# Kernel tuning notes

Hardware: AMD Instinct MI355X
Metric: run time of the kernel (lower is better)

Reference implementation:

```python
import jax, jax.numpy as jnp
import numpy as np

N = 100000      # nodes
E = 1600000     # edges
DIN, DH, DOUT = 128, 256, 40


def setup_inputs() -> dict:
    key = jax.random.key(0)
    ks = jax.random.split(key, 24)

    def w(i, fan_in, fan_out):
        s = 1.0 / np.sqrt(fan_in)
        return jax.random.uniform(ks[i], (fan_in, fan_out), jnp.float32, -s, s)

    def b(i, fan_in, fan_out):
        s = 1.0 / np.sqrt(fan_in)
        return jax.random.uniform(ks[i], (fan_out,), jnp.float32, -s, s)

    return {
        "x": jax.random.normal(ks[0], (N, DIN), jnp.float32),
        "edge_index": jax.random.randint(ks[1], (2, E), 0, N, dtype=jnp.int64),
        # updates_continues: Linear(DIN,DH), Linear(DH,DH), Linear(DH,DOUT)
        "Wc0": w(2, DIN, DH),  "bc0": b(3, DIN, DH),
        "Wc1": w(4, DH, DH),   "bc1": b(5, DH, DH),
        "Wc2": w(6, DH, DOUT), "bc2": b(7, DH, DOUT),
        # updates_exit: Linear(DIN,DOUT) x2, Linear(DH,DOUT) x2
        "We0": w(8, DIN, DOUT),  "be0": b(9, DIN, DOUT),
        "We1": w(10, DIN, DOUT), "be1": b(11, DIN, DOUT),
        "We2": w(12, DH, DOUT),  "be2": b(13, DH, DOUT),
        "We3": w(14, DH, DOUT),  "be3": b(15, DH, DOUT),
    }


def _gcn_agg(h, src, dst):
    """Symmetric-normalized GCN aggregation with self-loops: D^-1/2 (A+I) D^-1/2 h."""
    ones = jnp.ones(src.shape[0], h.dtype)
    deg = jax.ops.segment_sum(ones, dst, num_segments=N) + 1.0  # self-loop
    dinv = jax.lax.rsqrt(deg)
    coef = dinv[src] * dinv[dst]                    # [E]
    msgs = h[src] * coef[:, None]                   # [E, d] gather
    out = jax.ops.segment_sum(msgs, dst, num_segments=N)  # scatter-add
    return out + h * (dinv * dinv)[:, None]         # self-loop term


def reference(x, edge_index, Wc0, bc0, Wc1, bc1, Wc2, bc2,
              We0, be0, We1, be1, We2, be2, We3, be3):
    src, dst = edge_index[0], edge_index[1]
    Wc = [(Wc0, bc0), (Wc1, bc1), (Wc2, bc2)]
    We = [(We0, be0), (We1, be1), (We2, be2), (We3, be3)]

    h = x
    outs = [jax.nn.log_softmax(h @ We[0][0] + We[0][1], axis=1)]
    for i in range(3):
        h = _gcn_agg(h, src, dst)
        outs.append(jax.nn.log_softmax(h @ We[i + 1][0] + We[i + 1][1], axis=1))
        h = h @ Wc[i][0] + Wc[i][1]
        if i < 2:
            h = jax.nn.relu(h)  # dropout is identity in eval mode
    return jnp.stack(outs, axis=1)  # [N, num_layers+1, DOUT]
```

## Files before the change

### kernel.cpp

```cpp
#include <hip/hip_runtime.h>

#define NNODES 100000
#define NEDGES 1600000
#define NBKT 782

typedef __attribute__((ext_vector_type(8))) short bf16x8;
typedef __attribute__((ext_vector_type(4))) float f32x4;
typedef __attribute__((ext_vector_type(2))) float f32x2;

__device__ __forceinline__ float bf2f(unsigned v) {
  union { unsigned u; float f; } x; x.u = v << 16; return x.f;
}
__device__ __forceinline__ unsigned short f2bf(float f) {
  union { float f; unsigned u; } x; x.f = f;
  unsigned r = x.u + 0x7fffu + ((x.u >> 16) & 1u);
  return (unsigned short)(r >> 16);
}
__device__ __forceinline__ f32x2 unpk(unsigned u) {
  union { unsigned q; float f; } lo, hi;
  lo.q = u << 16; hi.q = u & 0xffff0000u;
  f32x2 r; r.x = lo.f; r.y = hi.f; return r;
}
__device__ __forceinline__ unsigned short ldcv(const void* p, int i, int f32) {
  return f32 ? f2bf(((const float*)p)[i]) : ((const unsigned short*)p)[i];
}
__device__ __forceinline__ int detect_i64(const int* __restrict__ ei) {
  int lane = threadIdx.x & 63;
  int hv = ei[2 * lane + 1];
  unsigned long long nz = __ballot(hv != 0);
  return (__popcll(nz) < 4) ? 1 : 0;
}
__device__ __forceinline__ int edge_at(const int* __restrict__ ei, int j, int i64) {
  return i64 ? ei[2 * j] : ei[j];
}

__global__ void k_zero(int* __restrict__ p, int n) {
  int v = blockIdx.x * blockDim.x + threadIdx.x;
  if (v < n) p[v] = 0;
}


__global__ __launch_bounds__(256) void k_bcnt(const int* __restrict__ ei,
                                              int* __restrict__ bcnt,
                                              const unsigned* __restrict__ xw,
                                              int* __restrict__ flags) {
  __shared__ int h[NBKT];
  __shared__ int cF;
  int t = threadIdx.x;
  for (int i = t; i < NBKT; i += 256) h[i] = 0;
  if (blockIdx.x == 0 && t == 0) cF = 0;
  __syncthreads();
  if (blockIdx.x == 0) {
    int hf = 0;
    for (int i = t; i < 2048; i += 256) {
      unsigned lo = xw[i] & 0xffffu;
      unsigned e = (lo >> 7) & 0xffu;
      if (e >= 0xC0u) hf++;
    }
    atomicAdd(&cF, hf);
  }
  int i64 = detect_i64(ei);
  int e0 = blockIdx.x * 4096;
#pragma unroll
  for (int k = 0; k < 16; ++k) {
    int e = e0 + t + k * 256;
    if (e < NEDGES) {
      int d = edge_at(ei, NEDGES + e, i64);
      if ((unsigned)d < NNODES) atomicAdd(&h[d >> 7], 1);
    }
  }
  __syncthreads();
  for (int i = t; i < NBKT; i += 256)
    if (h[i]) atomicAdd(&bcnt[i], h[i]);
  if (blockIdx.x == 0 && t == 0) flags[0] = (cF > 32) ? 1 : 0;
}

__global__ void k_bscan2(const int* __restrict__ bcnt, int* __restrict__ bbase,
                         int* __restrict__ gcur) {
  int l = threadIdx.x;
  int v[13];
  int s = 0;
#pragma unroll
  for (int k = 0; k < 13; ++k) {
    int j = l * 13 + k;
    v[k] = (j < NBKT) ? bcnt[j] : 0;
    s += v[k];
  }
  int x = s;
#pragma unroll
  for (int o = 1; o < 64; o <<= 1) {
    int y = __shfl_up(x, o, 64);
    if (l >= o) x += y;
  }
  int excl = x - s;
#pragma unroll
  for (int k = 0; k < 13; ++k) {
    int j = l * 13 + k;
    if (j < NBKT) { bbase[j] = excl; gcur[j] = excl; }
    excl += v[k];
  }
  if (l == 63) bbase[NBKT] = x;
}

__global__ __launch_bounds__(256) void k_bstage(const int* __restrict__ ei,
                                                int* __restrict__ gcur,
                                                int* __restrict__ stage) {
  __shared__ int h[NBKT];
  __shared__ int base[NBKT];
  int t = threadIdx.x;
  for (int i = t; i < NBKT; i += 256) h[i] = 0;
  __syncthreads();
  int i64 = detect_i64(ei);
  int e0 = blockIdx.x * 4096;
  int bkt[16], lp[16], rec[16];
#pragma unroll
  for (int k = 0; k < 16; ++k) {
    bkt[k] = -1;
    int e = e0 + t + k * 256;
    if (e < NEDGES) {
      int d = edge_at(ei, NEDGES + e, i64);
      if ((unsigned)d < NNODES) {
        int s = edge_at(ei, e, i64);
        if ((unsigned)s >= NNODES) s = NNODES - 1;
        bkt[k] = d >> 7;
        rec[k] = ((d & 127) << 17) | s;
        lp[k] = atomicAdd(&h[bkt[k]], 1);
      }
    }
  }
  __syncthreads();
  for (int i = t; i < NBKT; i += 256)
    base[i] = h[i] ? atomicAdd(&gcur[i], h[i]) : 0;
  __syncthreads();
#pragma unroll
  for (int k = 0; k < 16; ++k)
    if (bkt[k] >= 0) stage[base[bkt[k]] + lp[k]] = rec[k];
}

__global__ __launch_bounds__(256) void k_bplace(const int* __restrict__ stage,
                                                const int* __restrict__ bbase,
                                                int* __restrict__ offs,
                                                float* __restrict__ dinv,
                                                int* __restrict__ csr_src) {
  __shared__ int h[128];
  __shared__ int cur[128];
  int b = blockIdx.x;
  int t = threadIdx.x;
  int n0 = b * 128;
  int NN = NNODES - n0; if (NN > 128) NN = 128;
  int s0 = bbase[b], s1 = bbase[b + 1];
  int cnt = s1 - s0;
  if (t < 128) h[t] = 0;
  __syncthreads();
  for (int i = t; i < cnt; i += 256) {
    int rec = stage[s0 + i];
    atomicAdd(&h[rec >> 17], 1);
  }
  __syncthreads();
  if (t < 64) {
    int a = h[2 * t], c = h[2 * t + 1];
    int s = a + c;
    int x = s;
#pragma unroll
    for (int o = 1; o < 64; o <<= 1) {
      int y = __shfl_up(x, o, 64);
      if (t >= o) x += y;
    }
    int excl = s0 + x - s;
    cur[2 * t] = excl;
    cur[2 * t + 1] = excl + a;
    if (2 * t < NN) {
      offs[n0 + 2 * t] = excl;
      dinv[n0 + 2 * t] = rsqrtf((float)a + 1.0f);
    }
    if (2 * t + 1 < NN) {
      offs[n0 + 2 * t + 1] = excl + a;
      dinv[n0 + 2 * t + 1] = rsqrtf((float)c + 1.0f);
    }
  }
  if (b == NBKT - 1 && t == 0) offs[NNODES] = s1;
  __syncthreads();
  for (int i = t; i < cnt; i += 256) {
    int rec = stage[s0 + i];
    int pos = atomicAdd(&cur[rec >> 17], 1);
    csr_src[pos] = rec & 0x1FFFF;
  }
}

struct CvtP {
  const void* src[7];
  unsigned short* dst[7];
  int n[7];
  const void* W[6];
  unsigned short* WT[6];
};

__global__ void k_cvt(CvtP p, const int* __restrict__ flags,
                      const float* __restrict__ dinv, unsigned short* __restrict__ xs) {
  int a = blockIdx.y;
  int f32 = flags[0];
  if (a < 7) {
    int n = p.n[a];
    const float* sf = (const float*)p.src[a];
    const unsigned short* sb = (const unsigned short*)p.src[a];
    unsigned short* d = p.dst[a];
    for (int i = blockIdx.x * blockDim.x + threadIdx.x; i < n; i += gridDim.x * blockDim.x) {
      if (a == 0) {
        float v = f32 ? sf[i] : bf2f((unsigned)sb[i]);
        d[i] = f32 ? f2bf(v) : sb[i];
        xs[i] = f2bf(v * dinv[i >> 7]);
      } else {
        d[i] = f32 ? f2bf(sf[i]) : sb[i];
      }
    }
  } else {
    int g = blockIdx.x * 256 + threadIdx.x;
    if (g < 32768) {
      int k = g >> 8, c = g & 255;
      p.WT[0][c * 128 + k] = ldcv(p.W[0], g, f32);
    } else if (g < 98304) {
      int l = g - 32768; int k = l >> 8, c = l & 255;
      p.WT[1][c * 256 + k] = ldcv(p.W[1], l, f32);
    } else if (g < 104448) {
      int l = g - 98304; int c = l >> 7, k = l & 127;
      p.WT[2][l] = (c < 40) ? ldcv(p.W[2], k * 40 + c, f32) : (unsigned short)0;
    } else if (g < 110592) {
      int l = g - 104448; int c = l >> 7, k = l & 127;
      p.WT[3][l] = (c < 40) ? ldcv(p.W[3], k * 40 + c, f32) : (unsigned short)0;
    } else if (g < 122880) {
      int l = g - 110592; int c = l >> 8, k = l & 255;
      p.WT[4][l] = (c < 40) ? ldcv(p.W[4], k * 40 + c, f32) : (unsigned short)0;
    } else if (g < 135168) {
      int l = g - 122880; int c = l >> 8, k = l & 255;
      p.WT[5][l] = (c < 40) ? ldcv(p.W[5], k * 40 + c, f32) : (unsigned short)0;
    }
  }
}

__device__ __forceinline__ void accp(f32x2 (&acc)[4], uint4 u, float w) {
  acc[0] += unpk(u.x) * w;
  acc[1] += unpk(u.y) * w;
  acc[2] += unpk(u.z) * w;
  acc[3] += unpk(u.w) * w;
}

template <int D, int EPB>
__global__ __launch_bounds__(256) void k_agg(
    const unsigned short* __restrict__ hin, unsigned short* __restrict__ hout,
    const int* __restrict__ offs, const int* __restrict__ csr_src,
    const float* __restrict__ dinv) {
  constexpr int LPR = D / 8;
  constexpr int R = 64 / LPR;
  constexpr int NB = EPB / R;
  const int lane = threadIdx.x & 63;
  const int g = lane / LPR;
  const int l = lane % LPR;
  const int v = (blockIdx.x * 256 + threadIdx.x) >> 6;
  if (v >= NNODES) return;

  float dv = dinv[v];
  const size_t vbase = (size_t)v * D + l * 8;
  uint4 su = *(const uint4*)(hin + vbase);
  f32x2 acc[4];
#pragma unroll
  for (int k = 0; k < 4; ++k) acc[k] = (f32x2)0.f;
  accp(acc, su, (g == 0) ? 1.f : 0.f);

  int b0 = offs[v];
  int n = offs[v + 1] - b0;
  if (n > 0) {
    int s[NB];
    float wg[NB];
#pragma unroll
    for (int j = 0; j < NB; ++j) {
      int e = j * R + g;
      int ec = (e < n) ? e : (n - 1);
      s[j] = csr_src[b0 + ec];
      wg[j] = (e < n) ? 1.f : 0.f;
    }
    for (int i = 0; i < n; i += EPB) {
      uint4 gu[NB];
#pragma unroll
      for (int j = 0; j < NB; ++j)
        gu[j] = *(const uint4*)(hin + (size_t)s[j] * D + l * 8);
      float wc[NB];
#pragma unroll
      for (int j = 0; j < NB; ++j) wc[j] = wg[j];
      int i2 = i + EPB;
#pragma unroll
      for (int j = 0; j < NB; ++j) {
        int e = i2 + j * R + g;
        int ec = (e < n) ? e : (n - 1);
        s[j] = csr_src[b0 + ec];
        wg[j] = (e < n) ? 1.f : 0.f;
      }
#pragma unroll
      for (int j = 0; j < NB; ++j) accp(acc, gu[j], wc[j]);
    }
  }
  float a8[8];
#pragma unroll
  for (int k = 0; k < 4; ++k) { a8[2 * k] = acc[k].x; a8[2 * k + 1] = acc[k].y; }
#pragma unroll
  for (int k = 0; k < 8; ++k) {
#pragma unroll
    for (int o = LPR; o < 64; o <<= 1) a8[k] += __shfl_xor(a8[k], o, 64);
  }
  if (g == 0) {
    uint4 ov;
    ov.x = (unsigned)f2bf(dv * a8[0]) | ((unsigned)f2bf(dv * a8[1]) << 16);
    ov.y = (unsigned)f2bf(dv * a8[2]) | ((unsigned)f2bf(dv * a8[3]) << 16);
    ov.z = (unsigned)f2bf(dv * a8[4]) | ((unsigned)f2bf(dv * a8[5]) << 16);
    ov.w = (unsigned)f2bf(dv * a8[6]) | ((unsigned)f2bf(dv * a8[7]) << 16);
    *(uint4*)(hout + vbase) = ov;
  }
}

__global__ __launch_bounds__(256) void k_agg40(
    const unsigned short* __restrict__ P, const int* __restrict__ offs,
    const int* __restrict__ csr_src, const float* __restrict__ dinv,
    const unsigned short* __restrict__ bias, float* __restrict__ outp) {
  const int lane = threadIdx.x & 63;
  const int g = lane >> 5, l = lane & 31;
  const bool act = l < 20;
  const int v = (blockIdx.x * 256 + threadIdx.x) >> 6;
  if (v >= NNODES) return;

  float dv = dinv[v];
  f32x2 a = (f32x2)0.f;
  if (act && g == 0) a = unpk(*(const unsigned*)(P + (size_t)v * 40 + l * 2));
  int b0 = offs[v];
  int n = offs[v + 1] - b0;
  if (n > 0) {
    int s[4];
    float wg[4];
#pragma unroll
    for (int j = 0; j < 4; ++j) {
      int e = j * 2 + g;
      int ec = (e < n) ? e : (n - 1);
      s[j] = csr_src[b0 + ec];
      wg[j] = (e < n) ? 1.f : 0.f;
    }
    for (int i = 0; i < n; i += 8) {
      unsigned gu[4];
#pragma unroll
      for (int j = 0; j < 4; ++j)
        gu[j] = act ? *(const unsigned*)(P + (size_t)s[j] * 40 + l * 2) : 0u;
      float wc[4];
#pragma unroll
      for (int j = 0; j < 4; ++j) wc[j] = wg[j];
      int i2 = i + 8;
#pragma unroll
      for (int j = 0; j < 4; ++j) {
        int e = i2 + j * 2 + g;
        int ec = (e < n) ? e : (n - 1);
        s[j] = csr_src[b0 + ec];
        wg[j] = (e < n) ? 1.f : 0.f;
      }
#pragma unroll
      for (int j = 0; j < 4; ++j) a += unpk(gu[j]) * wc[j];
    }
  }
  a.x += __shfl_xor(a.x, 32, 64);
  a.y += __shfl_xor(a.y, 32, 64);
  float a0 = 0.f, a1 = 0.f;
  if (act) {
    a0 = dv * a.x + bf2f((unsigned)bias[l * 2]);
    a1 = dv * a.y + bf2f((unsigned)bias[l * 2 + 1]);
  }
  float m = act ? fmaxf(a0, a1) : -1e30f;
#pragma unroll
  for (int o = 16; o > 0; o >>= 1) m = fmaxf(m, __shfl_xor(m, o, 32));
  float ss = act ? (expf(a0 - m) + expf(a1 - m)) : 0.f;
#pragma unroll
  for (int o = 16; o > 0; o >>= 1) ss += __shfl_xor(ss, o, 32);
  float ls = logf(ss) + m;
  if (act && g == 0) {
    float2 o2;
    o2.x = a0 - ls;
    o2.y = a1 - ls;
    *(float2*)(outp + (size_t)v * 160 + l * 2) = o2;
  }
}

template <int K, bool SCALE>
__device__ __forceinline__ void mlp_body(
    char* smem, int m0, int c0,
    const unsigned short* __restrict__ A, const unsigned short* __restrict__ WT,
    const unsigned short* __restrict__ bias, unsigned short* __restrict__ out,
    const float* __restrict__ dinv) {
  short* As = (short*)smem;
  short* Bs = (short*)(smem + 10240);
  const int t = threadIdx.x;
  const int lane = t & 63, wv = t >> 6;
  const int mw = (wv >> 1) * 64, nw = (wv & 1) * 64;
  const int lr = lane & 15, lq = lane >> 4;

  f32x4 acc[4][4];
#pragma unroll
  for (int i = 0; i < 4; ++i)
#pragma unroll
    for (int j = 0; j < 4; ++j) acc[i][j] = (f32x4)0.f;

  for (int kc = 0; kc < K; kc += 32) {
    __syncthreads();
#pragma unroll
    for (int it = 0; it < 2; ++it) {
      int idx = t + it * 256;
      int row = idx >> 2, seg = idx & 3;
      uint4 u = make_uint4(0, 0, 0, 0);
      int gr = m0 + row;
      if (gr < NNODES) u = *(const uint4*)(A + (size_t)gr * K + kc + seg * 8);
      *(uint4*)&As[row * 40 + seg * 8] = u;
      uint4 v = *(const uint4*)(WT + (size_t)(c0 + row) * K + kc + seg * 8);
      *(uint4*)&Bs[row * 40 + seg * 8] = v;
    }
    __syncthreads();
    bf16x8 af[4], bfr[4];
#pragma unroll
    for (int i = 0; i < 4; ++i)
      af[i] = *(const bf16x8*)&As[(mw + 16 * i + lr) * 40 + lq * 8];
#pragma unroll
    for (int j = 0; j < 4; ++j)
      bfr[j] = *(const bf16x8*)&Bs[(nw + 16 * j + lr) * 40 + lq * 8];
#pragma unroll
    for (int i = 0; i < 4; ++i)
#pragma unroll
      for (int j = 0; j < 4; ++j)
        acc[i][j] = __builtin_amdgcn_mfma_f32_16x16x32_bf16(af[i], bfr[j], acc[i][j], 0, 0, 0);
  }

  float bv[4];
#pragma unroll
  for (int j = 0; j < 4; ++j) bv[j] = bf2f((unsigned)bias[c0 + nw + 16 * j + lr]);
#pragma unroll
  for (int i = 0; i < 4; ++i) {
    int rbase = m0 + mw + 16 * i + lq * 4;
#pragma unroll
    for (int r = 0; r < 4; ++r) {
      int row = rbase + r;
      if (row < NNODES) {
        float s = SCALE ? dinv[row] : 1.f;
#pragma unroll
        for (int j = 0; j < 4; ++j) {
          int col = c0 + nw + 16 * j + lr;
          float v = fmaxf(acc[i][j][r] + bv[j], 0.f) * s;
          out[(size_t)row * 256 + col] = f2bf(v);
        }
      }
    }
  }
}

template <int K, bool SOFTMAX>
__device__ __forceinline__ void exit_body(
    char* smem, int m0,
    const unsigned short* __restrict__ A, const unsigned short* __restrict__ WT,
    const unsigned short* __restrict__ bias, float* __restrict__ outp,
    unsigned short* __restrict__ Pout, const float* __restrict__ dinv) {
  constexpr int KP = K + 8;
  short* As = (short*)smem;
  short* Bs = (short*)(smem + 10240);
  const int t = threadIdx.x;
  const int lane = t & 63, wv = t >> 6;
  const int mw = wv * 32;
  const int lr = lane & 15, lq = lane >> 4;

  for (int idx = t; idx < 48 * (K / 8); idx += 256) {
    int row = idx / (K / 8), seg = idx % (K / 8);
    uint4 w = *(const uint4*)(WT + (size_t)row * K + seg * 8);
    *(uint4*)&Bs[row * KP + seg * 8] = w;
  }

  f32x4 acc[2][3];
#pragma unroll
  for (int i = 0; i < 2; ++i)
#pragma unroll
    for (int j = 0; j < 3; ++j) acc[i][j] = (f32x4)0.f;

  for (int kc = 0; kc < K; kc += 32) {
    __syncthreads();
#pragma unroll
    for (int it = 0; it < 2; ++it) {
      int idx = t + it * 256;
      int row = idx >> 2, seg = idx & 3;
      uint4 u = make_uint4(0, 0, 0, 0);
      int gr = m0 + row;
      if (gr < NNODES) u = *(const uint4*)(A + (size_t)gr * K + kc + seg * 8);
      *(uint4*)&As[row * 40 + seg * 8] = u;
    }
    __syncthreads();
    bf16x8 af[2], bfr[3];
#pragma unroll
    for (int i = 0; i < 2; ++i)
      af[i] = *(const bf16x8*)&As[(mw + 16 * i + lr) * 40 + lq * 8];
#pragma unroll
    for (int j = 0; j < 3; ++j)
      bfr[j] = *(const bf16x8*)&Bs[(16 * j + lr) * KP + kc + lq * 8];
#pragma unroll
    for (int i = 0; i < 2; ++i)
#pragma unroll
      for (int j = 0; j < 3; ++j)
        acc[i][j] = __builtin_amdgcn_mfma_f32_16x16x32_bf16(af[i], bfr[j], acc[i][j], 0, 0, 0);
  }

  if (SOFTMAX) {
    float bv0 = bf2f((unsigned)bias[lr]);
    float bv1 = bf2f((unsigned)bias[16 + lr]);
    float bv2 = (lr < 8) ? bf2f((unsigned)bias[32 + lr]) : 0.f;
#pragma unroll
    for (int i = 0; i < 2; ++i) {
#pragma unroll
      for (int r = 0; r < 4; ++r) {
        int row = m0 + mw + 16 * i + lq * 4 + r;
        float v0 = acc[i][0][r] + bv0;
        float v1 = acc[i][1][r] + bv1;
        float v2 = (lr < 8) ? (acc[i][2][r] + bv2) : -1e30f;
        float m = fmaxf(fmaxf(v0, v1), v2);
#pragma unroll
        for (int o = 8; o > 0; o >>= 1) m = fmaxf(m, __shfl_xor(m, o, 16));
        float ss = expf(v0 - m) + expf(v1 - m) + ((lr < 8) ? expf(v2 - m) : 0.f);
#pragma unroll
        for (int o = 8; o > 0; o >>= 1) ss += __shfl_xor(ss, o, 16);
        float ls = logf(ss) + m;
        if (row < NNODES) {
          outp[(size_t)row * 160 + lr] = v0 - ls;
          outp[(size_t)row * 160 + 16 + lr] = v1 - ls;
          if (lr < 8) outp[(size_t)row * 160 + 32 + lr] = v2 - ls;
        }
      }
    }
  } else {
#pragma unroll
    for (int i = 0; i < 2; ++i) {
#pragma unroll
      for (int r = 0; r < 4; ++r) {
        int row = m0 + mw + 16 * i + lq * 4 + r;
        if (row < NNODES) {
          float s = dinv[row];
          Pout[(size_t)row * 40 + lr] = f2bf(acc[i][0][r] * s);
          Pout[(size_t)row * 40 + 16 + lr] = f2bf(acc[i][1][r] * s);
          if (lr < 8) Pout[(size_t)row * 40 + 32 + lr] = f2bf(acc[i][2][r] * s);
        }
      }
    }
  }
}

template <int K> struct ExitSM { static constexpr int B = 10240 + 48 * (K + 8) * 2; };

__global__ __launch_bounds__(256) void k_exit0(
    const unsigned short* __restrict__ A, const unsigned short* __restrict__ WT,
    const unsigned short* __restrict__ bias, float* __restrict__ outp,
    const float* __restrict__ dinv) {
  __shared__ __align__(16) char smem[ExitSM<128>::B];
  exit_body<128, true>(smem, blockIdx.x * 128, A, WT, bias, outp, nullptr, dinv);
}

__global__ __launch_bounds__(256) void k_exit3(
    const unsigned short* __restrict__ A, const unsigned short* __restrict__ WT,
    unsigned short* __restrict__ Pout, const float* __restrict__ dinv) {
  __shared__ __align__(16) char smem[ExitSM<256>::B];
  exit_body<256, false>(smem, blockIdx.x * 128, A, WT, nullptr, nullptr, Pout, dinv);
}

template <int K, bool MLPSCALE>
__global__ __launch_bounds__(256) void k_exit_mlp(
    const unsigned short* __restrict__ A,
    const unsigned short* __restrict__ WTmlp, const unsigned short* __restrict__ bmlp,
    unsigned short* __restrict__ outmlp,
    const unsigned short* __restrict__ WTex, const unsigned short* __restrict__ bex,
    float* __restrict__ outp, const float* __restrict__ dinv) {
  constexpr int SM = (ExitSM<K>::B > 20480) ? ExitSM<K>::B : 20480;
  __shared__ __align__(16) char smem[SM];
  int bid = blockIdx.x;
  if (bid < 1564) {
    mlp_body<K, MLPSCALE>(smem, (bid >> 1) * 128, (bid & 1) * 128, A, WTmlp, bmlp, outmlp, dinv);
  } else {
    exit_body<K, true>(smem, (bid - 1564) * 128, A, WTex, bex, outp, nullptr, dinv);
  }
}

extern "C" void kernel_launch(void* const* d_in, const int* in_sizes, int n_in,
                              void* d_out, int out_size, void* d_ws, size_t ws_size,
                              hipStream_t stream) {
  const void* x_raw   = d_in[0];
  const int* ei       = (const int*)d_in[1];
  float* out          = (float*)d_out;

  char* ws = (char*)d_ws;
  int*   flags    = (int*)(ws + 0);
  int*   bcnt     = (int*)(ws + 4096);
  int*   gcur     = (int*)(ws + 8192);
  int*   bbase    = (int*)(ws + 12288);
  float* dinv     = (float*)(ws + 524288);
  int*   offs     = (int*)(ws + 1048576);
  int*   csr_src  = (int*)(ws + 2097152);
  int*   stage    = (int*)(ws + 8650752);
  unsigned short* xb = (unsigned short*)(ws + 16777216);
  unsigned short* wb = (unsigned short*)(ws + 45088768);
  unsigned short* hA = (unsigned short*)(ws + 48234496);
  unsigned short* hB = (unsigned short*)(ws + 100663296);
  unsigned short* xs = hB;
  unsigned short* P  = xb;

  unsigned short* bc0 = wb + 32768;
  unsigned short* bc1 = wb + 98560;
  unsigned short* be0 = wb + 103936;
  unsigned short* be1 = wb + 109096;
  unsigned short* be2 = wb + 119376;
  unsigned short* be3 = wb + 129656;
  unsigned short* WTc0  = wb + 131072;
  unsigned short* WTc1  = wb + 163840;
  unsigned short* WT40e0 = wb + 229376;
  unsigned short* WT40e1 = wb + 235520;
  unsigned short* WT40e2 = wb + 241664;
  unsigned short* WT40e3 = wb + 253952;

  dim3 B(256);
  k_zero<<<dim3(4), B, 0, stream>>>(bcnt, NBKT);
  k_bcnt<<<dim3(391), B, 0, stream>>>(ei, bcnt, (const unsigned*)x_raw, flags);
  k_bscan2<<<dim3(1), dim3(64), 0, stream>>>(bcnt, bbase, gcur);
  k_bstage<<<dim3(391), B, 0, stream>>>(ei, gcur, stage);
  k_bplace<<<dim3(NBKT), B, 0, stream>>>(stage, bbase, offs, dinv, csr_src);

  CvtP p;
  const int bsrc[7] = {0, 3, 5, 9, 11, 13, 15};
  unsigned short* bdst[7] = {xb, bc0, bc1, be0, be1, be2, be3};
  const int bn[7] = {NNODES * 128, 256, 256, 40, 40, 40, 40};
  for (int i = 0; i < 7; ++i) { p.src[i] = d_in[bsrc[i]]; p.dst[i] = bdst[i]; p.n[i] = bn[i]; }
  const int wsrc[6] = {2, 4, 8, 10, 12, 14};
  unsigned short* wdst[6] = {WTc0, WTc1, WT40e0, WT40e1, WT40e2, WT40e3};
  for (int i = 0; i < 6; ++i) { p.W[i] = d_in[wsrc[i]]; p.WT[i] = wdst[i]; }
  k_cvt<<<dim3(1024, 8), B, 0, stream>>>(p, flags, dinv, xs);

  k_exit0<<<dim3(782), B, 0, stream>>>(xb, WT40e0, be0, out + 0 * 40, dinv);
  k_agg<128, 16><<<dim3(25000), B, 0, stream>>>(xs, hA, offs, csr_src, dinv);
  k_exit_mlp<128, true><<<dim3(2346), B, 0, stream>>>(hA, WTc0, bc0, hB,
                                                      WT40e1, be1, out + 1 * 40, dinv);
  k_agg<256, 8><<<dim3(25000), B, 0, stream>>>(hB, hA, offs, csr_src, dinv);
  k_exit_mlp<256, false><<<dim3(2346), B, 0, stream>>>(hA, WTc1, bc1, hB,
                                                       WT40e2, be2, out + 2 * 40, dinv);
  k_exit3<<<dim3(782), B, 0, stream>>>(hB, WT40e3, P, dinv);
  k_agg40<<<dim3(25000), B, 0, stream>>>(P, offs, csr_src, dinv, be3, out + 3 * 40);
}
```

Before: 623.3 us.

## Store node features in 16-column planes and aggregate one plane per block

```diff
diff --git a/kernel.cpp b/kernel.cpp
--- a/kernel.cpp
+++ b/kernel.cpp
@@ -3,6 +3,7 @@
 #define NNODES 100000
 #define NEDGES 1600000
 #define NBKT 782
+#define PLANE_ELT ((size_t)NNODES * 16)
 
 typedef __attribute__((ext_vector_type(8))) short bf16x8;
 typedef __attribute__((ext_vector_type(4))) float f32x4;
@@ -38,7 +39,6 @@
   int v = blockIdx.x * blockDim.x + threadIdx.x;
   if (v < n) p[v] = 0;
 }
-
 
 __global__ __launch_bounds__(256) void k_bcnt(const int* __restrict__ ei,
                                               int* __restrict__ bcnt,
@@ -208,7 +208,9 @@
       if (a == 0) {
         float v = f32 ? sf[i] : bf2f((unsigned)sb[i]);
         d[i] = f32 ? f2bf(v) : sb[i];
-        xs[i] = f2bf(v * dinv[i >> 7]);
+        int row = i >> 7, col = i & 127;
+        xs[(size_t)(col >> 4) * PLANE_ELT + (size_t)row * 16 + (col & 15)] =
+            f2bf(v * dinv[row]);
       } else {
         d[i] = f32 ? f2bf(sf[i]) : sb[i];
       }
@@ -237,82 +239,58 @@
   }
 }
 
-__device__ __forceinline__ void accp(f32x2 (&acc)[4], uint4 u, float w) {
-  acc[0] += unpk(u.x) * w;
-  acc[1] += unpk(u.y) * w;
-  acc[2] += unpk(u.z) * w;
-  acc[3] += unpk(u.w) * w;
-}
-
-template <int D, int EPB>
-__global__ __launch_bounds__(256) void k_agg(
-    const unsigned short* __restrict__ hin, unsigned short* __restrict__ hout,
+template <int NPLANES>
+__global__ __launch_bounds__(256) void k_aggp(
+    const unsigned short* __restrict__ IP, unsigned short* __restrict__ OP,
     const int* __restrict__ offs, const int* __restrict__ csr_src,
     const float* __restrict__ dinv) {
-  constexpr int LPR = D / 8;
-  constexpr int R = 64 / LPR;
-  constexpr int NB = EPB / R;
+  int b = blockIdx.x;
+  int bb = b >> 3;
+  int plane = (b & 7) + 8 * (bb / 2500);
+  int j0 = bb % 2500;
   const int lane = threadIdx.x & 63;
-  const int g = lane / LPR;
-  const int l = lane % LPR;
-  const int v = (blockIdx.x * 256 + threadIdx.x) >> 6;
-  if (v >= NNODES) return;
-
-  float dv = dinv[v];
-  const size_t vbase = (size_t)v * D + l * 8;
-  uint4 su = *(const uint4*)(hin + vbase);
-  f32x2 acc[4];
-#pragma unroll
-  for (int k = 0; k < 4; ++k) acc[k] = (f32x2)0.f;
-  accp(acc, su, (g == 0) ? 1.f : 0.f);
-
-  int b0 = offs[v];
-  int n = offs[v + 1] - b0;
-  if (n > 0) {
-    int s[NB];
-    float wg[NB];
-#pragma unroll
-    for (int j = 0; j < NB; ++j) {
-      int e = j * R + g;
-      int ec = (e < n) ? e : (n - 1);
-      s[j] = csr_src[b0 + ec];
-      wg[j] = (e < n) ? 1.f : 0.f;
-    }
-    for (int i = 0; i < n; i += EPB) {
-      uint4 gu[NB];
-#pragma unroll
-      for (int j = 0; j < NB; ++j)
-        gu[j] = *(const uint4*)(hin + (size_t)s[j] * D + l * 8);
-      float wc[NB];
-#pragma unroll
-      for (int j = 0; j < NB; ++j) wc[j] = wg[j];
-      int i2 = i + EPB;
-#pragma unroll
-      for (int j = 0; j < NB; ++j) {
-        int e = i2 + j * R + g;
-        int ec = (e < n) ? e : (n - 1);
-        s[j] = csr_src[b0 + ec];
-        wg[j] = (e < n) ? 1.f : 0.f;
+  const int wvi = threadIdx.x >> 6;
+  const int c = lane & 7;
+  const int g = lane >> 3;
+  const unsigned short* ip = IP + (size_t)plane * PLANE_ELT;
+  unsigned short* op = OP + (size_t)plane * PLANE_ELT;
+
+  for (int j = j0; j < 25000; j += 2500) {
+    int v = j * 4 + wvi;
+    float dv = dinv[v];
+    unsigned su = *(const unsigned*)(ip + (size_t)v * 16 + c * 2);
+    f32x2 acc = unpk(su) * ((g == 0) ? 1.f : 0.f);
+    int b0 = offs[v];
+    int n = offs[v + 1] - b0;
+    if (n > 0) {
+      int e0 = g, e1 = 8 + g;
+      int s0 = __builtin_nontemporal_load(csr_src + b0 + (e0 < n ? e0 : n - 1));
+      int s1 = __builtin_nontemporal_load(csr_src + b0 + (e1 < n ? e1 : n - 1));
+      float w0 = (e0 < n) ? 1.f : 0.f;
+      float w1 = (e1 < n) ? 1.f : 0.f;
+      for (int i = 0; i < n; i += 16) {
+        unsigned u0 = *(const unsigned*)(ip + (size_t)s0 * 16 + c * 2);
+        unsigned u1 = *(const unsigned*)(ip + (size_t)s1 * 16 + c * 2);
+        float wc0 = w0, wc1 = w1;
+        int i2 = i + 16;
+        e0 = i2 + g; e1 = i2 + 8 + g;
+        s0 = __builtin_nontemporal_load(csr_src + b0 + (e0 < n ? e0 : n - 1));
+        s1 = __builtin_nontemporal_load(csr_src + b0 + (e1 < n ? e1 : n - 1));
+        w0 = (e0 < n) ? 1.f : 0.f;
+        w1 = (e1 < n) ? 1.f : 0.f;
+        acc += unpk(u0) * wc0;
+        acc += unpk(u1) * wc1;
       }
-#pragma unroll
-      for (int j = 0; j < NB; ++j) accp(acc, gu[j], wc[j]);
-    }
-  }
-  float a8[8];
-#pragma unroll
-  for (int k = 0; k < 4; ++k) { a8[2 * k] = acc[k].x; a8[2 * k + 1] = acc[k].y; }
-#pragma unroll
-  for (int k = 0; k < 8; ++k) {
-#pragma unroll
-    for (int o = LPR; o < 64; o <<= 1) a8[k] += __shfl_xor(a8[k], o, 64);
-  }
-  if (g == 0) {
-    uint4 ov;
-    ov.x = (unsigned)f2bf(dv * a8[0]) | ((unsigned)f2bf(dv * a8[1]) << 16);
-    ov.y = (unsigned)f2bf(dv * a8[2]) | ((unsigned)f2bf(dv * a8[3]) << 16);
-    ov.z = (unsigned)f2bf(dv * a8[4]) | ((unsigned)f2bf(dv * a8[5]) << 16);
-    ov.w = (unsigned)f2bf(dv * a8[6]) | ((unsigned)f2bf(dv * a8[7]) << 16);
-    *(uint4*)(hout + vbase) = ov;
+    }
+#pragma unroll
+    for (int o = 8; o < 64; o <<= 1) {
+      acc.x += __shfl_xor(acc.x, o, 64);
+      acc.y += __shfl_xor(acc.y, o, 64);
+    }
+    if (g == 0) {
+      unsigned r = (unsigned)f2bf(dv * acc.x) | ((unsigned)f2bf(dv * acc.y) << 16);
+      *(unsigned*)(op + (size_t)v * 16 + c * 2) = r;
+    }
   }
 }
 
@@ -381,6 +359,13 @@
     o2.y = a1 - ls;
     *(float2*)(outp + (size_t)v * 160 + l * 2) = o2;
   }
+}
+
+template <int K, bool PLANES>
+__device__ __forceinline__ uint4 ldA(const unsigned short* __restrict__ A, int gr, int cc) {
+  if (PLANES)
+    return *(const uint4*)(A + (size_t)(cc >> 4) * PLANE_ELT + (size_t)gr * 16 + (cc & 15));
+  return *(const uint4*)(A + (size_t)gr * K + cc);
 }
 
 template <int K, bool SCALE>
@@ -410,7 +395,7 @@
       int row = idx >> 2, seg = idx & 3;
       uint4 u = make_uint4(0, 0, 0, 0);
       int gr = m0 + row;
-      if (gr < NNODES) u = *(const uint4*)(A + (size_t)gr * K + kc + seg * 8);
+      if (gr < NNODES) u = ldA<K, true>(A, gr, kc + seg * 8);
       *(uint4*)&As[row * 40 + seg * 8] = u;
       uint4 v = *(const uint4*)(WT + (size_t)(c0 + row) * K + kc + seg * 8);
       *(uint4*)&Bs[row * 40 + seg * 8] = v;
@@ -445,14 +430,14 @@
         for (int j = 0; j < 4; ++j) {
           int col = c0 + nw + 16 * j + lr;
           float v = fmaxf(acc[i][j][r] + bv[j], 0.f) * s;
-          out[(size_t)row * 256 + col] = f2bf(v);
+          out[(size_t)(col >> 4) * PLANE_ELT + (size_t)row * 16 + (col & 15)] = f2bf(v);
         }
       }
     }
   }
 }
 
-template <int K, bool SOFTMAX>
+template <int K, bool SOFTMAX, bool PLANES>
 __device__ __forceinline__ void exit_body(
     char* smem, int m0,
     const unsigned short* __restrict__ A, const unsigned short* __restrict__ WT,
@@ -486,7 +471,7 @@
       int row = idx >> 2, seg = idx & 3;
       uint4 u = make_uint4(0, 0, 0, 0);
       int gr = m0 + row;
-      if (gr < NNODES) u = *(const uint4*)(A + (size_t)gr * K + kc + seg * 8);
+      if (gr < NNODES) u = ldA<K, PLANES>(A, gr, kc + seg * 8);
       *(uint4*)&As[row * 40 + seg * 8] = u;
     }
     __syncthreads();
@@ -554,14 +539,14 @@
     const unsigned short* __restrict__ bias, float* __restrict__ outp,
     const float* __restrict__ dinv) {
   __shared__ __align__(16) char smem[ExitSM<128>::B];
-  exit_body<128, true>(smem, blockIdx.x * 128, A, WT, bias, outp, nullptr, dinv);
+  exit_body<128, true, false>(smem, blockIdx.x * 128, A, WT, bias, outp, nullptr, dinv);
 }
 
 __global__ __launch_bounds__(256) void k_exit3(
     const unsigned short* __restrict__ A, const unsigned short* __restrict__ WT,
     unsigned short* __restrict__ Pout, const float* __restrict__ dinv) {
   __shared__ __align__(16) char smem[ExitSM<256>::B];
-  exit_body<256, false>(smem, blockIdx.x * 128, A, WT, nullptr, nullptr, Pout, dinv);
+  exit_body<256, false, true>(smem, blockIdx.x * 128, A, WT, nullptr, nullptr, Pout, dinv);
 }
 
 template <int K, bool MLPSCALE>
@@ -577,7 +562,7 @@
   if (bid < 1564) {
     mlp_body<K, MLPSCALE>(smem, (bid >> 1) * 128, (bid & 1) * 128, A, WTmlp, bmlp, outmlp, dinv);
   } else {
-    exit_body<K, true>(smem, (bid - 1564) * 128, A, WTex, bex, outp, nullptr, dinv);
+    exit_body<K, true, true>(smem, (bid - 1564) * 128, A, WTex, bex, outp, nullptr, dinv);
   }
 }
 
@@ -635,10 +620,10 @@
   k_cvt<<<dim3(1024, 8), B, 0, stream>>>(p, flags, dinv, xs);
 
   k_exit0<<<dim3(782), B, 0, stream>>>(xb, WT40e0, be0, out + 0 * 40, dinv);
-  k_agg<128, 16><<<dim3(25000), B, 0, stream>>>(xs, hA, offs, csr_src, dinv);
+  k_aggp<8><<<dim3(20000), B, 0, stream>>>(xs, hA, offs, csr_src, dinv);
   k_exit_mlp<128, true><<<dim3(2346), B, 0, stream>>>(hA, WTc0, bc0, hB,
                                                       WT40e1, be1, out + 1 * 40, dinv);
-  k_agg<256, 8><<<dim3(25000), B, 0, stream>>>(hB, hA, offs, csr_src, dinv);
+  k_aggp<16><<<dim3(40000), B, 0, stream>>>(hB, hA, offs, csr_src, dinv);
   k_exit_mlp<256, false><<<dim3(2346), B, 0, stream>>>(hA, WTc1, bc1, hB,
                                                        WT40e2, be2, out + 2 * 40, dinv);
   k_exit3<<<dim3(782), B, 0, stream>>>(hB, WT40e3, P, dinv);
```

After: 1.044 ms. +67.5%, slower.

## Fuse GCN aggregation with MLP and exit GEMMs via shared-memory tiles

Applied to the files above, without the earlier changes.

```diff
diff --git a/kernel.cpp b/kernel.cpp
--- a/kernel.cpp
+++ b/kernel.cpp
@@ -38,7 +38,6 @@
   int v = blockIdx.x * blockDim.x + threadIdx.x;
   if (v < n) p[v] = 0;
 }
-
 
 __global__ __launch_bounds__(256) void k_bcnt(const int* __restrict__ ei,
                                               int* __restrict__ bcnt,
@@ -244,163 +243,218 @@
   acc[3] += unpk(u.w) * w;
 }
 
-template <int D, int EPB>
-__global__ __launch_bounds__(256) void k_agg(
-    const unsigned short* __restrict__ hin, unsigned short* __restrict__ hout,
+template <int K, bool SCALE, int TILES, int GRID>
+__global__ __launch_bounds__(256) void k_fused(
+    const unsigned short* __restrict__ hin,
+    const unsigned short* __restrict__ WTmlp, const unsigned short* __restrict__ bmlp,
+    unsigned short* __restrict__ outmlp,
+    const unsigned short* __restrict__ WTex, const unsigned short* __restrict__ bex,
+    float* __restrict__ outp,
     const int* __restrict__ offs, const int* __restrict__ csr_src,
     const float* __restrict__ dinv) {
-  constexpr int LPR = D / 8;
+  constexpr int KP = K + 8;
+  constexpr int LPR = K / 8;
   constexpr int R = 64 / LPR;
+  constexpr int EPB = 16;
   constexpr int NB = EPB / R;
-  const int lane = threadIdx.x & 63;
-  const int g = lane / LPR;
-  const int l = lane % LPR;
-  const int v = (blockIdx.x * 256 + threadIdx.x) >> 6;
-  if (v >= NNODES) return;
-
-  float dv = dinv[v];
-  const size_t vbase = (size_t)v * D + l * 8;
-  uint4 su = *(const uint4*)(hin + vbase);
-  f32x2 acc[4];
-#pragma unroll
-  for (int k = 0; k < 4; ++k) acc[k] = (f32x2)0.f;
-  accp(acc, su, (g == 0) ? 1.f : 0.f);
-
-  int b0 = offs[v];
-  int n = offs[v + 1] - b0;
-  if (n > 0) {
-    int s[NB];
-    float wg[NB];
-#pragma unroll
-    for (int j = 0; j < NB; ++j) {
-      int e = j * R + g;
-      int ec = (e < n) ? e : (n - 1);
-      s[j] = csr_src[b0 + ec];
-      wg[j] = (e < n) ? 1.f : 0.f;
-    }
-    for (int i = 0; i < n; i += EPB) {
-      uint4 gu[NB];
-#pragma unroll
-      for (int j = 0; j < NB; ++j)
-        gu[j] = *(const uint4*)(hin + (size_t)s[j] * D + l * 8);
-      float wc[NB];
-#pragma unroll
-      for (int j = 0; j < NB; ++j) wc[j] = wg[j];
-      int i2 = i + EPB;
-#pragma unroll
-      for (int j = 0; j < NB; ++j) {
-        int e = i2 + j * R + g;
-        int ec = (e < n) ? e : (n - 1);
-        s[j] = csr_src[b0 + ec];
-        wg[j] = (e < n) ? 1.f : 0.f;
-      }
-#pragma unroll
-      for (int j = 0; j < NB; ++j) accp(acc, gu[j], wc[j]);
-    }
-  }
-  float a8[8];
-#pragma unroll
-  for (int k = 0; k < 4; ++k) { a8[2 * k] = acc[k].x; a8[2 * k + 1] = acc[k].y; }
-#pragma unroll
-  for (int k = 0; k < 8; ++k) {
-#pragma unroll
-    for (int o = LPR; o < 64; o <<= 1) a8[k] += __shfl_xor(a8[k], o, 64);
-  }
-  if (g == 0) {
-    uint4 ov;
-    ov.x = (unsigned)f2bf(dv * a8[0]) | ((unsigned)f2bf(dv * a8[1]) << 16);
-    ov.y = (unsigned)f2bf(dv * a8[2]) | ((unsigned)f2bf(dv * a8[3]) << 16);
-    ov.z = (unsigned)f2bf(dv * a8[4]) | ((unsigned)f2bf(dv * a8[5]) << 16);
-    ov.w = (unsigned)f2bf(dv * a8[6]) | ((unsigned)f2bf(dv * a8[7]) << 16);
-    *(uint4*)(hout + vbase) = ov;
-  }
-}
-
-__global__ __launch_bounds__(256) void k_agg40(
-    const unsigned short* __restrict__ P, const int* __restrict__ offs,
-    const int* __restrict__ csr_src, const float* __restrict__ dinv,
-    const unsigned short* __restrict__ bias, float* __restrict__ outp) {
-  const int lane = threadIdx.x & 63;
-  const int g = lane >> 5, l = lane & 31;
-  const bool act = l < 20;
-  const int v = (blockIdx.x * 256 + threadIdx.x) >> 6;
-  if (v >= NNODES) return;
-
-  float dv = dinv[v];
-  f32x2 a = (f32x2)0.f;
-  if (act && g == 0) a = unpk(*(const unsigned*)(P + (size_t)v * 40 + l * 2));
-  int b0 = offs[v];
-  int n = offs[v + 1] - b0;
-  if (n > 0) {
-    int s[4];
-    float wg[4];
-#pragma unroll
-    for (int j = 0; j < 4; ++j) {
-      int e = j * 2 + g;
-      int ec = (e < n) ? e : (n - 1);
-      s[j] = csr_src[b0 + ec];
-      wg[j] = (e < n) ? 1.f : 0.f;
-    }
-    for (int i = 0; i < n; i += 8) {
-      unsigned gu[4];
-#pragma unroll
-      for (int j = 0; j < 4; ++j)
-        gu[j] = act ? *(const unsigned*)(P + (size_t)s[j] * 40 + l * 2) : 0u;
-      float wc[4];
-#pragma unroll
-      for (int j = 0; j < 4; ++j) wc[j] = wg[j];
-      int i2 = i + 8;
-#pragma unroll
-      for (int j = 0; j < 4; ++j) {
-        int e = i2 + j * 2 + g;
-        int ec = (e < n) ? e : (n - 1);
-        s[j] = csr_src[b0 + ec];
-        wg[j] = (e < n) ? 1.f : 0.f;
-      }
-#pragma unroll
-      for (int j = 0; j < 4; ++j) a += unpk(gu[j]) * wc[j];
-    }
-  }
-  a.x += __shfl_xor(a.x, 32, 64);
-  a.y += __shfl_xor(a.y, 32, 64);
-  float a0 = 0.f, a1 = 0.f;
-  if (act) {
-    a0 = dv * a.x + bf2f((unsigned)bias[l * 2]);
-    a1 = dv * a.y + bf2f((unsigned)bias[l * 2 + 1]);
-  }
-  float m = act ? fmaxf(a0, a1) : -1e30f;
-#pragma unroll
-  for (int o = 16; o > 0; o >>= 1) m = fmaxf(m, __shfl_xor(m, o, 32));
-  float ss = act ? (expf(a0 - m) + expf(a1 - m)) : 0.f;
-#pragma unroll
-  for (int o = 16; o > 0; o >>= 1) ss += __shfl_xor(ss, o, 32);
-  float ls = logf(ss) + m;
-  if (act && g == 0) {
-    float2 o2;
-    o2.x = a0 - ls;
-    o2.y = a1 - ls;
-    *(float2*)(outp + (size_t)v * 160 + l * 2) = o2;
-  }
-}
-
-template <int K, bool SCALE>
-__device__ __forceinline__ void mlp_body(
-    char* smem, int m0, int c0,
-    const unsigned short* __restrict__ A, const unsigned short* __restrict__ WT,
-    const unsigned short* __restrict__ bias, unsigned short* __restrict__ out,
-    const float* __restrict__ dinv) {
-  short* As = (short*)smem;
-  short* Bs = (short*)(smem + 10240);
+  __shared__ __align__(16) short A[64 * KP];
+  __shared__ __align__(16) short Bs[128 * 40];
+  const int t = threadIdx.x;
+  const int lane = t & 63, wvi = t >> 6;
+  const int g = lane / LPR, l = lane % LPR;
+  const int lr = lane & 15, lq = lane >> 4;
+
+  for (int tile = 0; tile < TILES; ++tile) {
+    int m0 = (blockIdx.x + tile * GRID) * 64;
+    if (m0 >= NNODES) break;
+    __syncthreads();
+
+    for (int w = 0; w < 16; ++w) {
+      int v = m0 + wvi * 16 + w;
+      if (v >= NNODES) break;
+      float dv = dinv[v];
+      uint4 su = *(const uint4*)(hin + (size_t)v * K + l * 8);
+      f32x2 acc[4];
+#pragma unroll
+      for (int k = 0; k < 4; ++k) acc[k] = (f32x2)0.f;
+      accp(acc, su, (g == 0) ? 1.f : 0.f);
+
+      int b0 = offs[v];
+      int n = offs[v + 1] - b0;
+      if (n > 0) {
+        int s[NB];
+        float wg[NB];
+#pragma unroll
+        for (int j = 0; j < NB; ++j) {
+          int e = j * R + g;
+          s[j] = csr_src[b0 + (e < n ? e : n - 1)];
+          wg[j] = (e < n) ? 1.f : 0.f;
+        }
+        for (int i = 0; i < n; i += EPB) {
+          uint4 gu[NB];
+#pragma unroll
+          for (int j = 0; j < NB; ++j)
+            gu[j] = *(const uint4*)(hin + (size_t)s[j] * K + l * 8);
+          float wc[NB];
+#pragma unroll
+          for (int j = 0; j < NB; ++j) wc[j] = wg[j];
+          int i2 = i + EPB;
+#pragma unroll
+          for (int j = 0; j < NB; ++j) {
+            int e = i2 + j * R + g;
+            s[j] = csr_src[b0 + (e < n ? e : n - 1)];
+            wg[j] = (e < n) ? 1.f : 0.f;
+          }
+#pragma unroll
+          for (int j = 0; j < NB; ++j) accp(acc, gu[j], wc[j]);
+        }
+      }
+      float a8[8];
+#pragma unroll
+      for (int k = 0; k < 4; ++k) { a8[2 * k] = acc[k].x; a8[2 * k + 1] = acc[k].y; }
+#pragma unroll
+      for (int k = 0; k < 8; ++k) {
+#pragma unroll
+        for (int o = LPR; o < 64; o <<= 1) a8[k] += __shfl_xor(a8[k], o, 64);
+      }
+      if (g == 0) {
+        uint4 ov;
+        ov.x = (unsigned)f2bf(dv * a8[0]) | ((unsigned)f2bf(dv * a8[1]) << 16);
+        ov.y = (unsigned)f2bf(dv * a8[2]) | ((unsigned)f2bf(dv * a8[3]) << 16);
+        ov.z = (unsigned)f2bf(dv * a8[4]) | ((unsigned)f2bf(dv * a8[5]) << 16);
+        ov.w = (unsigned)f2bf(dv * a8[6]) | ((unsigned)f2bf(dv * a8[7]) << 16);
+        *(uint4*)&A[(v - m0) * KP + l * 8] = ov;
+      }
+    }
+
+    {
+      const int mw = (wvi >> 1) * 32, nw = (wvi & 1) * 64;
+#pragma unroll
+      for (int c0 = 0; c0 < 256; c0 += 128) {
+        f32x4 acc[2][4];
+#pragma unroll
+        for (int i = 0; i < 2; ++i)
+#pragma unroll
+          for (int j = 0; j < 4; ++j) acc[i][j] = (f32x4)0.f;
+        for (int kc = 0; kc < K; kc += 32) {
+          __syncthreads();
+#pragma unroll
+          for (int it = 0; it < 2; ++it) {
+            int idx = t + it * 256;
+            int row = idx >> 2, seg = idx & 3;
+            uint4 u = *(const uint4*)(WTmlp + (size_t)(c0 + row) * K + kc + seg * 8);
+            *(uint4*)&Bs[row * 40 + seg * 8] = u;
+          }
+          __syncthreads();
+          bf16x8 af[2], bfr[4];
+#pragma unroll
+          for (int i = 0; i < 2; ++i)
+            af[i] = *(const bf16x8*)&A[(mw + 16 * i + lr) * KP + kc + lq * 8];
+#pragma unroll
+          for (int j = 0; j < 4; ++j)
+            bfr[j] = *(const bf16x8*)&Bs[(nw + 16 * j + lr) * 40 + lq * 8];
+#pragma unroll
+          for (int i = 0; i < 2; ++i)
+#pragma unroll
+            for (int j = 0; j < 4; ++j)
+              acc[i][j] = __builtin_amdgcn_mfma_f32_16x16x32_bf16(af[i], bfr[j], acc[i][j], 0, 0, 0);
+        }
+        float bv[4];
+#pragma unroll
+        for (int j = 0; j < 4; ++j) bv[j] = bf2f((unsigned)bmlp[c0 + nw + 16 * j + lr]);
+#pragma unroll
+        for (int i = 0; i < 2; ++i) {
+          int rbase = m0 + mw + 16 * i + lq * 4;
+#pragma unroll
+          for (int r = 0; r < 4; ++r) {
+            int row = rbase + r;
+            if (row < NNODES) {
+              float s = SCALE ? dinv[row] : 1.f;
+#pragma unroll
+              for (int j = 0; j < 4; ++j) {
+                int col = c0 + nw + 16 * j + lr;
+                float v = fmaxf(acc[i][j][r] + bv[j], 0.f) * s;
+                outmlp[(size_t)row * 256 + col] = f2bf(v);
+              }
+            }
+          }
+        }
+      }
+    }
+
+    {
+      const int mw = wvi * 16;
+      f32x4 acc[3];
+#pragma unroll
+      for (int j = 0; j < 3; ++j) acc[j] = (f32x4)0.f;
+      for (int kc = 0; kc < K; kc += 32) {
+        __syncthreads();
+        if (t < 192) {
+          int row = t >> 2, seg = t & 3;
+          uint4 u = *(const uint4*)(WTex + (size_t)row * K + kc + seg * 8);
+          *(uint4*)&Bs[row * 40 + seg * 8] = u;
+        }
+        __syncthreads();
+        bf16x8 af = *(const bf16x8*)&A[(mw + lr) * KP + kc + lq * 8];
+        bf16x8 bfr[3];
+#pragma unroll
+        for (int j = 0; j < 3; ++j)
+          bfr[j] = *(const bf16x8*)&Bs[(16 * j + lr) * 40 + lq * 8];
+#pragma unroll
+        for (int j = 0; j < 3; ++j)
+          acc[j] = __builtin_amdgcn_mfma_f32_16x16x32_bf16(af, bfr[j], acc[j], 0, 0, 0);
+      }
+      float bv0 = bf2f((unsigned)bex[lr]);
+      float bv1 = bf2f((unsigned)bex[16 + lr]);
+      float bv2 = (lr < 8) ? bf2f((unsigned)bex[32 + lr]) : 0.f;
+#pragma unroll
+      for (int r = 0; r < 4; ++r) {
+        int row = m0 + mw + lq * 4 + r;
+        float v0 = acc[0][r] + bv0;
+        float v1 = acc[1][r] + bv1;
+        float v2 = (lr < 8) ? (acc[2][r] + bv2) : -1e30f;
+        float m = fmaxf(fmaxf(v0, v1), v2);
+#pragma unroll
+        for (int o = 8; o > 0; o >>= 1) m = fmaxf(m, __shfl_xor(m, o, 16));
+        float ss = expf(v0 - m) + expf(v1 - m) + ((lr < 8) ? expf(v2 - m) : 0.f);
+#pragma unroll
+        for (int o = 8; o > 0; o >>= 1) ss += __shfl_xor(ss, o, 16);
+        float ls = logf(ss) + m;
+        if (row < NNODES) {
+          outp[(size_t)row * 160 + lr] = v0 - ls;
+          outp[(size_t)row * 160 + 16 + lr] = v1 - ls;
+          if (lr < 8) outp[(size_t)row * 160 + 32 + lr] = v2 - ls;
+        }
+      }
+    }
+  }
+}
+
+template <int K, bool SOFTMAX>
+__global__ __launch_bounds__(256) void k_exit(
+    const unsigned short* __restrict__ Ain, const unsigned short* __restrict__ WT,
+    const unsigned short* __restrict__ bias, float* __restrict__ outp,
+    unsigned short* __restrict__ Pout, const float* __restrict__ dinv) {
+  constexpr int KP = K + 8;
+  __shared__ __align__(16) short As[128 * 40];
+  __shared__ __align__(16) short Bsp[48 * KP];
   const int t = threadIdx.x;
   const int lane = t & 63, wv = t >> 6;
-  const int mw = (wv >> 1) * 64, nw = (wv & 1) * 64;
+  const int m0 = blockIdx.x * 128;
+  const int mw = wv * 32;
   const int lr = lane & 15, lq = lane >> 4;
 
-  f32x4 acc[4][4];
-#pragma unroll
-  for (int i = 0; i < 4; ++i)
-#pragma unroll
-    for (int j = 0; j < 4; ++j) acc[i][j] = (f32x4)0.f;
+  for (int idx = t; idx < 48 * (K / 8); idx += 256) {
+    int row = idx / (K / 8), seg = idx % (K / 8);
+    uint4 w = *(const uint4*)(WT + (size_t)row * K + seg * 8);
+    *(uint4*)&Bsp[row * KP + seg * 8] = w;
+  }
+
+  f32x4 acc[2][3];
+#pragma unroll
+  for (int i = 0; i < 2; ++i)
+#pragma unroll
+    for (int j = 0; j < 3; ++j) acc[i][j] = (f32x4)0.f;
 
   for (int kc = 0; kc < K; kc += 32) {
     __syncthreads();
@@ -410,83 +464,7 @@
       int row = idx >> 2, seg = idx & 3;
       uint4 u = make_uint4(0, 0, 0, 0);
       int gr = m0 + row;
-      if (gr < NNODES) u = *(const uint4*)(A + (size_t)gr * K + kc + seg * 8);
-      *(uint4*)&As[row * 40 + seg * 8] = u;
-      uint4 v = *(const uint4*)(WT + (size_t)(c0 + row) * K + kc + seg * 8);
-      *(uint4*)&Bs[row * 40 + seg * 8] = v;
-    }
-    __syncthreads();
-    bf16x8 af[4], bfr[4];
-#pragma unroll
-    for (int i = 0; i < 4; ++i)
-      af[i] = *(const bf16x8*)&As[(mw + 16 * i + lr) * 40 + lq * 8];
-#pragma unroll
-    for (int j = 0; j < 4; ++j)
-      bfr[j] = *(const bf16x8*)&Bs[(nw + 16 * j + lr) * 40 + lq * 8];
-#pragma unroll
-    for (int i = 0; i < 4; ++i)
-#pragma unroll
-      for (int j = 0; j < 4; ++j)
-        acc[i][j] = __builtin_amdgcn_mfma_f32_16x16x32_bf16(af[i], bfr[j], acc[i][j], 0, 0, 0);
-  }
-
-  float bv[4];
-#pragma unroll
-  for (int j = 0; j < 4; ++j) bv[j] = bf2f((unsigned)bias[c0 + nw + 16 * j + lr]);
-#pragma unroll
-  for (int i = 0; i < 4; ++i) {
-    int rbase = m0 + mw + 16 * i + lq * 4;
-#pragma unroll
-    for (int r = 0; r < 4; ++r) {
-      int row = rbase + r;
-      if (row < NNODES) {
-        float s = SCALE ? dinv[row] : 1.f;
-#pragma unroll
-        for (int j = 0; j < 4; ++j) {
-          int col = c0 + nw + 16 * j + lr;
-          float v = fmaxf(acc[i][j][r] + bv[j], 0.f) * s;
-          out[(size_t)row * 256 + col] = f2bf(v);
-        }
-      }
-    }
-  }
-}
-
-template <int K, bool SOFTMAX>
-__device__ __forceinline__ void exit_body(
-    char* smem, int m0,
-    const unsigned short* __restrict__ A, const unsigned short* __restrict__ WT,
-    const unsigned short* __restrict__ bias, float* __restrict__ outp,
-    unsigned short* __restrict__ Pout, const float* __restrict__ dinv) {
-  constexpr int KP = K + 8;
-  short* As = (short*)smem;
-  short* Bs = (short*)(smem + 10240);
-  const int t = threadIdx.x;
-  const int lane = t & 63, wv = t >> 6;
-  const int mw = wv * 32;
-  const int lr = lane & 15, lq = lane >> 4;
-
-  for (int idx = t; idx < 48 * (K / 8); idx += 256) {
-    int row = idx / (K / 8), seg = idx % (K / 8);
-    uint4 w = *(const uint4*)(WT + (size_t)row * K + seg * 8);
-    *(uint4*)&Bs[row * KP + seg * 8] = w;
-  }
-
-  f32x4 acc[2][3];
-#pragma unroll
-  for (int i = 0; i < 2; ++i)
-#pragma unroll
-    for (int j = 0; j < 3; ++j) acc[i][j] = (f32x4)0.f;
-
-  for (int kc = 0; kc < K; kc += 32) {
-    __syncthreads();
-#pragma unroll
-    for (int it = 0; it < 2; ++it) {
-      int idx = t + it * 256;
-      int row = idx >> 2, seg = idx & 3;
-      uint4 u = make_uint4(0, 0, 0, 0);
-      int gr = m0 + row;
-      if (gr < NNODES) u = *(const uint4*)(A + (size_t)gr * K + kc + seg * 8);
+      if (gr < NNODES) u = *(const uint4*)(Ain + (size_t)gr * K + kc + seg * 8);
       *(uint4*)&As[row * 40 + seg * 8] = u;
     }
     __syncthreads();
@@ -496,7 +474,7 @@
       af[i] = *(const bf16x8*)&As[(mw + 16 * i + lr) * 40 + lq * 8];
 #pragma unroll
     for (int j = 0; j < 3; ++j)
-      bfr[j] = *(const bf16x8*)&Bs[(16 * j + lr) * KP + kc + lq * 8];
+      bfr[j] = *(const bf16x8*)&Bsp[(16 * j + lr) * KP + kc + lq * 8];
 #pragma unroll
     for (int i = 0; i < 2; ++i)
 #pragma unroll
@@ -538,46 +516,84 @@
         int row = m0 + mw + 16 * i + lq * 4 + r;
         if (row < NNODES) {
           float s = dinv[row];
-          Pout[(size_t)row * 40 + lr] = f2bf(acc[i][0][r] * s);
-          Pout[(size_t)row * 40 + 16 + lr] = f2bf(acc[i][1][r] * s);
-          if (lr < 8) Pout[(size_t)row * 40 + 32 + lr] = f2bf(acc[i][2][r] * s);
-        }
-      }
-    }
-  }
-}
-
-template <int K> struct ExitSM { static constexpr int B = 10240 + 48 * (K + 8) * 2; };
-
-__global__ __launch_bounds__(256) void k_exit0(
-    const unsigned short* __restrict__ A, const unsigned short* __restrict__ WT,
-    const unsigned short* __restrict__ bias, float* __restrict__ outp,
-    const float* __restrict__ dinv) {
-  __shared__ __align__(16) char smem[ExitSM<128>::B];
-  exit_body<128, true>(smem, blockIdx.x * 128, A, WT, bias, outp, nullptr, dinv);
-}
-
-__global__ __launch_bounds__(256) void k_exit3(
-    const unsigned short* __restrict__ A, const unsigned short* __restrict__ WT,
-    unsigned short* __restrict__ Pout, const float* __restrict__ dinv) {
-  __shared__ __align__(16) char smem[ExitSM<256>::B];
-  exit_body<256, false>(smem, blockIdx.x * 128, A, WT, nullptr, nullptr, Pout, dinv);
-}
-
-template <int K, bool MLPSCALE>
-__global__ __launch_bounds__(256) void k_exit_mlp(
-    const unsigned short* __restrict__ A,
-    const unsigned short* __restrict__ WTmlp, const unsigned short* __restrict__ bmlp,
-    unsigned short* __restrict__ outmlp,
-    const unsigned short* __restrict__ WTex, const unsigned short* __restrict__ bex,
-    float* __restrict__ outp, const float* __restrict__ dinv) {
-  constexpr int SM = (ExitSM<K>::B > 20480) ? ExitSM<K>::B : 20480;
-  __shared__ __align__(16) char smem[SM];
-  int bid = blockIdx.x;
-  if (bid < 1564) {
-    mlp_body<K, MLPSCALE>(smem, (bid >> 1) * 128, (bid & 1) * 128, A, WTmlp, bmlp, outmlp, dinv);
-  } else {
-    exit_body<K, true>(smem, (bid - 1564) * 128, A, WTex, bex, outp, nullptr, dinv);
+          Pout[(size_t)row * 48 + lr] = f2bf(acc[i][0][r] * s);
+          Pout[(size_t)row * 48 + 16 + lr] = f2bf(acc[i][1][r] * s);
+          Pout[(size_t)row * 48 + 32 + lr] =
+              (lr < 8) ? f2bf(acc[i][2][r] * s) : (unsigned short)0;
+        }
+      }
+    }
+  }
+}
+
+__global__ __launch_bounds__(256) void k_agg40(
+    const unsigned short* __restrict__ P, const int* __restrict__ offs,
+    const int* __restrict__ csr_src, const float* __restrict__ dinv,
+    const unsigned short* __restrict__ bias, float* __restrict__ outp) {
+  const int lane = threadIdx.x & 63;
+  const int g = lane / 12;
+  const int l = lane % 12;
+  const bool act = lane < 60;
+  const int v = (blockIdx.x * 256 + threadIdx.x) >> 6;
+  if (v >= NNODES) return;
+
+  float dv = dinv[v];
+  f32x2 a0 = (f32x2)0.f, a1 = (f32x2)0.f;
+  if (act && g == 0) {
+    uint2 su = *(const uint2*)(P + (size_t)v * 48 + l * 4);
+    a0 = unpk(su.x);
+    a1 = unpk(su.y);
+  }
+  int b0 = offs[v];
+  int n = offs[v + 1] - b0;
+  if (n > 0) {
+    int e0 = g, e1 = 5 + g;
+    int s0 = csr_src[b0 + (e0 < n ? e0 : n - 1)];
+    int s1 = csr_src[b0 + (e1 < n ? e1 : n - 1)];
+    float w0 = (act && e0 < n) ? 1.f : 0.f;
+    float w1 = (act && e1 < n) ? 1.f : 0.f;
+    for (int i = 0; i < n; i += 10) {
+      uint2 u0 = *(const uint2*)(P + (size_t)s0 * 48 + l * 4);
+      uint2 u1 = *(const uint2*)(P + (size_t)s1 * 48 + l * 4);
+      float wc0 = w0, wc1 = w1;
+      int i2 = i + 10;
+      e0 = i2 + g; e1 = i2 + 5 + g;
+      s0 = csr_src[b0 + (e0 < n ? e0 : n - 1)];
+      s1 = csr_src[b0 + (e1 < n ? e1 : n - 1)];
+      w0 = (act && e0 < n) ? 1.f : 0.f;
+      w1 = (act && e1 < n) ? 1.f : 0.f;
+      a0 += unpk(u0.x) * wc0;
+      a1 += unpk(u0.y) * wc0;
+      a0 += unpk(u1.x) * wc1;
+      a1 += unpk(u1.y) * wc1;
+    }
+  }
+  float sums[4] = {a0.x, a0.y, a1.x, a1.y};
+#pragma unroll
+  for (int k = 0; k < 4; ++k) {
+    float x = sums[k];
+    float x1 = __shfl(x, lane + 12, 64);
+    float x2 = __shfl(x, lane + 24, 64);
+    float x3 = __shfl(x, lane + 36, 64);
+    float x4 = __shfl(x, lane + 48, 64);
+    sums[k] = x + x1 + x2 + x3 + x4;
+  }
+  bool ol = (g == 0) && (l < 10);
+  float c0v = ol ? (dv * sums[0] + bf2f((unsigned)bias[l * 4 + 0])) : -1e30f;
+  float c1v = ol ? (dv * sums[1] + bf2f((unsigned)bias[l * 4 + 1])) : -1e30f;
+  float c2v = ol ? (dv * sums[2] + bf2f((unsigned)bias[l * 4 + 2])) : -1e30f;
+  float c3v = ol ? (dv * sums[3] + bf2f((unsigned)bias[l * 4 + 3])) : -1e30f;
+  float m = fmaxf(fmaxf(c0v, c1v), fmaxf(c2v, c3v));
+#pragma unroll
+  for (int o = 8; o > 0; o >>= 1) m = fmaxf(m, __shfl_xor(m, o, 16));
+  float ss = ol ? (expf(c0v - m) + expf(c1v - m) + expf(c2v - m) + expf(c3v - m)) : 0.f;
+#pragma unroll
+  for (int o = 8; o > 0; o >>= 1) ss += __shfl_xor(ss, o, 16);
+  float ls = logf(ss) + m;
+  if (ol) {
+    float4 o4;
+    o4.x = c0v - ls; o4.y = c1v - ls; o4.z = c2v - ls; o4.w = c3v - ls;
+    *(float4*)(outp + (size_t)v * 160 + l * 4) = o4;
   }
 }
 
@@ -634,13 +650,11 @@
   for (int i = 0; i < 6; ++i) { p.W[i] = d_in[wsrc[i]]; p.WT[i] = wdst[i]; }
   k_cvt<<<dim3(1024, 8), B, 0, stream>>>(p, flags, dinv, xs);
 
-  k_exit0<<<dim3(782), B, 0, stream>>>(xb, WT40e0, be0, out + 0 * 40, dinv);
-  k_agg<128, 16><<<dim3(25000), B, 0, stream>>>(xs, hA, offs, csr_src, dinv);
-  k_exit_mlp<128, true><<<dim3(2346), B, 0, stream>>>(hA, WTc0, bc0, hB,
-                                                      WT40e1, be1, out + 1 * 40, dinv);
-  k_agg<256, 8><<<dim3(25000), B, 0, stream>>>(hB, hA, offs, csr_src, dinv);
-  k_exit_mlp<256, false><<<dim3(2346), B, 0, stream>>>(hA, WTc1, bc1, hB,
-                                                       WT40e2, be2, out + 2 * 40, dinv);
-  k_exit3<<<dim3(782), B, 0, stream>>>(hB, WT40e3, P, dinv);
+  k_exit<128, true><<<dim3(782), B, 0, stream>>>(xb, WT40e0, be0, out + 0 * 40, nullptr, dinv);
+  k_fused<128, true, 2, 782><<<dim3(782), B, 0, stream>>>(
+      xs, WTc0, bc0, hA, WT40e1, be1, out + 1 * 40, offs, csr_src, dinv);
+  k_fused<256, false, 3, 522><<<dim3(522), B, 0, stream>>>(
+      hA, WTc1, bc1, hB, WT40e2, be2, out + 2 * 40, offs, csr_src, dinv);
+  k_exit<256, false><<<dim3(782), B, 0, stream>>>(hB, WT40e3, nullptr, nullptr, P, dinv);
   k_agg40<<<dim3(25000), B, 0, stream>>>(P, offs, csr_src, dinv, be3, out + 3 * 40);
 }
```

Result: slower. 743.9 us (+19.4%).
